# Kernel tuning notes

Hardware: AMD Instinct MI355X
Metric: run time of the kernel (lower is better)

## Reference

```python
import jax, jax.numpy as jnp
import numpy as np
from jax import lax

E = 8          # num_experts
L1 = 1024      # input feature dim
L2 = 15        # hidden 1 (l1 outputs L2+1, last channel is residual)
L3 = 32        # hidden 2
RF = 32        # router features per perspective
AUX_ALPHA = 0.01
Z_ALPHA = 0.001
LOAD_FLOOR = 0.05
LOAD_CAP = 0.5
TEACHER_ALPHA = 0.5  # _teacher_alpha buffer (epoch 0, no annealing)


def setup_inputs() -> dict:
    key = jax.random.key(0)
    ks = jax.random.split(key, 12)
    B = 32768
    s = 0.05
    return {
        "x": jax.random.normal(ks[0], (B, L1), dtype=jnp.float32),
        "ls_indices": jax.random.randint(ks[1], (B,), 0, E),
        "router_w": jax.random.normal(ks[2], (E, 2 * RF), dtype=jnp.float32) * 0.1,
        "router_b": jnp.zeros((E,), dtype=jnp.float32),
        "l1_w": jax.random.normal(ks[3], (E * (L2 + 1), L1), dtype=jnp.float32) * s,
        "l1_fw": jax.random.normal(ks[4], (L2 + 1, L1), dtype=jnp.float32) * s,
        "l1_b": jax.random.normal(ks[5], (E * (L2 + 1),), dtype=jnp.float32) * s,
        "l1_fb": jax.random.normal(ks[6], (L2 + 1,), dtype=jnp.float32) * s,
        "l2_w": jax.random.normal(ks[7], (E * L3, 2 * L2), dtype=jnp.float32) * s,
        "l2_b": jax.random.normal(ks[8], (E * L3,), dtype=jnp.float32) * s,
        "out_w": jax.random.normal(ks[9], (E * 1, L3), dtype=jnp.float32) * s,
        "out_b": jnp.zeros((E * 1,), dtype=jnp.float32),
    }


def _forward(x, ls_indices, router_w, router_b, l1_w, l1_fw, l1_b, l1_fb,
             l2_w, l2_b, out_w, out_b):
    B = x.shape[0]
    half = x.shape[1] // 2

    # ---- router ----
    router_input = jnp.concatenate([x[:, :RF], x[:, half:half + RF]], axis=1)  # (B, 64)
    gate_logits = router_input @ router_w.T + router_b                          # (B, E)
    logp = jax.nn.log_softmax(gate_logits, axis=-1)
    gate_probs = jnp.exp(logp)
    expert_indices = jnp.argmax(gate_logits, axis=-1)                           # (B,)

    target_prob = jnp.take_along_axis(gate_probs, ls_indices[:, None], axis=1).mean()
    bucket_agreement = (expert_indices == ls_indices).astype(gate_probs.dtype).mean()
    teacher_ce = -jnp.take_along_axis(logp, ls_indices[:, None], axis=1).mean()

    fraction_routed = jnp.bincount(expert_indices, length=E).astype(gate_probs.dtype) / B
    avg_gate_prob = gate_probs.mean(axis=0)
    load_estimate = avg_gate_prob + lax.stop_gradient(fraction_routed - avg_gate_prob)
    load_floor_loss = jnp.square(jax.nn.relu(LOAD_FLOOR - load_estimate)).mean()
    load_cap_loss = jnp.square(jax.nn.relu(load_estimate - LOAD_CAP)).mean()
    aux_loss = load_floor_loss + load_cap_loss
    z_loss = jnp.square(jax.scipy.special.logsumexp(gate_logits, axis=-1)).mean()
    router_loss = AUX_ALPHA * aux_loss + Z_ALPHA * z_loss + TEACHER_ALPHA * teacher_ce

    # ---- all-experts MLP (3 batched GEMMs, clamp/square fusion path) ----
    w1 = (l1_w + jnp.tile(l1_fw, (E, 1))).reshape(E, L2 + 1, L1)
    b1 = (l1_b + jnp.tile(l1_fb, E)).reshape(E, L2 + 1)
    w2 = l2_w.reshape(E, L3, 2 * L2)
    b2 = l2_b.reshape(E, L3)
    w3 = out_w.reshape(E, 1, L3)
    b3 = out_b.reshape(E, 1)

    l1c = jnp.einsum('bi,eoi->beo', x, w1) + b1          # (B, E, L2+1)
    l1x, l1x_out = l1c[..., :L2], l1c[..., L2:]          # (B,E,L2), (B,E,1)
    act = jnp.clip(jnp.concatenate([l1x * l1x * (255.0 / 256.0), l1x], axis=2), 0.0, 1.0)
    l2c = jnp.einsum('bei,eoi->beo', act, w2) + b2       # (B, E, L3)
    l2x = jnp.clip(l2c, 0.0, 1.0)
    l3c = jnp.einsum('bei,eoi->beo', l2x, w3) + b3       # (B, E, 1)
    all_out = l3c + l1x_out                              # (B, E, 1)

    # route by argmax expert
    sel = jnp.take_along_axis(all_out, expert_indices[:, None, None], axis=1).squeeze(1)  # (B,1)
    # training-mode straight-through gate scaling (value-preserving)
    gate_prob = jnp.take_along_axis(gate_probs, expert_indices[:, None], axis=1)
    sel = sel * (1.0 + gate_prob - lax.stop_gradient(gate_prob))

    return (sel, router_loss, aux_loss, z_loss, teacher_ce,
            fraction_routed, avg_gate_prob, target_prob, bucket_agreement)


def reference(x, ls_indices, router_w, router_b, l1_w, l1_fw, l1_b, l1_fb,
              l2_w, l2_b, out_w, out_b):
    return _forward(x, ls_indices, router_w, router_b, l1_w, l1_fw, l1_b, l1_fb,
                    l2_w, l2_b, out_w, out_b)
```

## Files before the change

kernel.cpp:

```cpp
#include <hip/hip_runtime.h>
#include <math.h>


#define NE 8
#define NL1 1024
#define NB 32768
#define NCH 512
#define NTOK 32

#define WS_W1C    0
#define WS_B1C    131072
#define WS_COUNTS 131200
#define WS_PART   131208
#define WS_PMAX   132744
#define WS_SORTED 165512

typedef __attribute__((ext_vector_type(4))) float f32x4;
typedef __attribute__((ext_vector_type(8))) short bf16x8;
typedef __attribute__((ext_vector_type(4))) unsigned u32x4;

__device__ __forceinline__ float clamp01(float v) { return fminf(fmaxf(v, 0.0f), 1.0f); }

__device__ __forceinline__ bf16x8 cvt8(float4 lo, float4 hi) {
  unsigned p0, p1, p2, p3;
  asm("v_cvt_pk_bf16_f32 %0, %1, %2" : "=v"(p0) : "v"(lo.x), "v"(lo.y));
  asm("v_cvt_pk_bf16_f32 %0, %1, %2" : "=v"(p1) : "v"(lo.z), "v"(lo.w));
  asm("v_cvt_pk_bf16_f32 %0, %1, %2" : "=v"(p2) : "v"(hi.x), "v"(hi.y));
  asm("v_cvt_pk_bf16_f32 %0, %1, %2" : "=v"(p3) : "v"(hi.z), "v"(hi.w));
  u32x4 u; u.x = p0; u.y = p1; u.z = p2; u.w = p3;
  return __builtin_bit_cast(bf16x8, u);
}

__global__ __launch_bounds__(256) void k_prep(const float* __restrict__ l1_w,
                                              const float* __restrict__ l1_fw,
                                              const float* __restrict__ l1_b,
                                              const float* __restrict__ l1_fb,
                                              float* __restrict__ ws) {
  const int r = blockIdx.x;
  const int t = threadIdx.x;
  const float* src  = l1_w + r * NL1;
  const float* fsrc = l1_fw + (r & 15) * NL1;
  float* dst = ws + WS_W1C + r * NL1;
#pragma unroll
  for (int k = 0; k < 4; ++k) {
    const int i = t + k * 256;
    dst[i] = src[i] + fsrc[i];
  }
  if (r == 0) {
    if (t < 128) ws[WS_B1C + t] = l1_b[t] + l1_fb[t & 15];
    if (t >= 128 && t < 136) ((int*)ws)[WS_COUNTS + (t - 128)] = 0;
  }
}

__device__ __forceinline__ float wsum(float v) {
#pragma unroll
  for (int m = 32; m >= 1; m >>= 1) v += __shfl_xor(v, m, 64);
  return v;
}

__global__ __launch_bounds__(256) void k_router(const float* __restrict__ x,
                                                const int* __restrict__ ls,
                                                const float* __restrict__ rw,
                                                const float* __restrict__ rb,
                                                float* __restrict__ ws) {
  __shared__ float part[4][12];
  __shared__ int hist[NE];
  __shared__ int hbase[NE];
  const int t = threadIdx.x;
  const int w = t >> 6;
  const int b = blockIdx.x * 256 + t;
  if (t < NE) hist[t] = 0;
  __syncthreads();

  float ri[64];
  const float4* xr = (const float4*)(x + (size_t)b * NL1);
#pragma unroll
  for (int q = 0; q < 8; ++q) {
    float4 v = xr[q];
    ri[q * 4 + 0] = v.x; ri[q * 4 + 1] = v.y; ri[q * 4 + 2] = v.z; ri[q * 4 + 3] = v.w;
  }
#pragma unroll
  for (int q = 0; q < 8; ++q) {
    float4 v = xr[128 + q];
    ri[32 + q * 4 + 0] = v.x; ri[32 + q * 4 + 1] = v.y; ri[32 + q * 4 + 2] = v.z; ri[32 + q * 4 + 3] = v.w;
  }

  float logits[NE];
#pragma unroll
  for (int e = 0; e < NE; ++e) {
    float s = rb[e];
    const float* wv = rw + e * 64;
#pragma unroll
    for (int k = 0; k < 64; ++k) s = fmaf(ri[k], wv[k], s);
    logits[e] = s;
  }

  float m = logits[0]; int am = 0;
#pragma unroll
  for (int e = 1; e < NE; ++e) { if (logits[e] > m) { m = logits[e]; am = e; } }
  float se = 0.0f;
#pragma unroll
  for (int e = 0; e < NE; ++e) se += expf(logits[e] - m);
  const float lse = m + logf(se);
  float p[NE];
#pragma unroll
  for (int e = 0; e < NE; ++e) p[e] = expf(logits[e] - lse);

  const int lsb = ls[b];
  float tp = 0.0f, lls = 0.0f, psel = 0.0f;
#pragma unroll
  for (int e = 0; e < NE; ++e) {
    tp   = (e == lsb) ? p[e] : tp;
    lls  = (e == lsb) ? logits[e] : lls;
    psel = (e == am)  ? p[e] : psel;
  }
  const float agree = (am == lsb) ? 1.0f : 0.0f;
  const float tce = lse - lls;
  const float z = lse * lse;

  ws[WS_PMAX + b] = psel;

  int* wsI = (int*)ws;
  const int lpos = atomicAdd(&hist[am], 1);

  const float sA = wsum(tp), sB = wsum(agree), sC = wsum(tce), sD = wsum(z);
  const float q0 = wsum(p[0]), q1 = wsum(p[1]), q2 = wsum(p[2]), q3 = wsum(p[3]);
  const float q4 = wsum(p[4]), q5 = wsum(p[5]), q6 = wsum(p[6]), q7 = wsum(p[7]);
  if ((t & 63) == 0) {
    part[w][0] = sA; part[w][1] = sB; part[w][2]  = sC; part[w][3]  = sD;
    part[w][4] = q0; part[w][5] = q1; part[w][6]  = q2; part[w][7]  = q3;
    part[w][8] = q4; part[w][9] = q5; part[w][10] = q6; part[w][11] = q7;
  }
  __syncthreads();
  if (t < 12) ws[WS_PART + blockIdx.x * 12 + t] =
      (part[0][t] + part[1][t]) + (part[2][t] + part[3][t]);
  if (t < NE) hbase[t] = atomicAdd(&wsI[WS_COUNTS + t], hist[t]);
  __syncthreads();
  wsI[WS_SORTED + am * NB + hbase[am] + lpos] = b;
}

__global__ void k_finalize(const float* __restrict__ ws, float* __restrict__ out) {
  __shared__ float red[12][16];
  const int t = threadIdx.x;
  if (t < 192) {
    const int s = t >> 4, j = t & 15;
    float v = 0.0f;
#pragma unroll
    for (int m = 0; m < 8; ++m) v += ws[WS_PART + (j + 16 * m) * 12 + s];
    red[s][j] = v;
  }
  __syncthreads();
  if (t == 0) {
    float st[12];
#pragma unroll
    for (int s = 0; s < 12; ++s) {
      float v = 0.0f;
#pragma unroll
      for (int j = 0; j < 16; ++j) v += red[s][j];
      st[s] = v;
    }
    const float invB = 1.0f / 32768.0f;
    const int* wsI = (const int*)ws;
    float aux_floor = 0.0f, aux_cap = 0.0f;
#pragma unroll
    for (int e = 0; e < NE; ++e) {
      const float frac = (float)wsI[WS_COUNTS + e] * invB;
      const float avg  = st[4 + e] * invB;
      const float le = avg + (frac - avg);
      const float f = fmaxf(0.05f - le, 0.0f);
      const float c = fmaxf(le - 0.5f, 0.0f);
      aux_floor += f * f;
      aux_cap   += c * c;
      out[32772 + e] = frac;
      out[32780 + e] = avg;
    }
    const float aux = aux_floor * 0.125f + aux_cap * 0.125f;
    const float zl  = st[3] * invB;
    const float tce = st[2] * invB;
    out[32768] = 0.01f * aux + 0.001f * zl + 0.5f * tce;
    out[32769] = aux;
    out[32770] = zl;
    out[32771] = tce;
    out[32788] = st[0] * invB;
    out[32789] = st[1] * invB;
  }
}

__global__ __launch_bounds__(256) void k_expert(const float* __restrict__ x,
                                                const float* __restrict__ ws,
                                                const float* __restrict__ l2_w,
                                                const float* __restrict__ l2_b,
                                                const float* __restrict__ out_w,
                                                const float* __restrict__ out_b,
                                                float* __restrict__ out) {
  __shared__ float lds[8192];
  const int t = threadIdx.x;
  const int l = t & 63;
  const int w = t >> 6;
  const int bid = blockIdx.x;
  const int e = bid >> 9;
  const int c = bid & 511;
  const int* wsI = (const int*)ws;
  const int n = wsI[WS_COUNTS + e];
  const int start = c * NTOK;
  if (start >= n) return;

  const int g = l >> 4;
  const int r0 = l & 15;
  const int r1 = r0 + 16;

  const float* We = ws + WS_W1C + e * 16 * NL1;
  const float* Wr = We + r0 * NL1 + 256 * w + 8 * g;
  bf16x8 bfrag[8];
#pragma unroll
  for (int st2 = 0; st2 < 8; ++st2) {
    const float4 blo = *(const float4*)&Wr[32 * st2];
    const float4 bhi = *(const float4*)&Wr[32 * st2 + 4];
    bfrag[st2] = cvt8(blo, bhi);
  }

  const int lam = l & 31;
  const int lh  = l >> 5;
  const float* srcp[4];
#pragma unroll
  for (int j = 0; j < 4; ++j) {
    const int tl = 8 * w + 2 * j + lh;
    int pos = start + tl; if (pos > n - 1) pos = n - 1;
    const int tokid = wsI[WS_SORTED + e * NB + pos];
    const int cc = (4 * lam) ^ (tl << 2);
    srcp[j] = x + (size_t)tokid * NL1 + 256 * (cc >> 5) + (cc & 31);
  }

  const int q0 = (8 * w + 2 * g) ^ r0;
  const int q1 = (8 * w + 2 * g) ^ r1;
  const int a0lo = r0 * 128 + 4 * q0,        a0hi = r0 * 128 + 4 * (q0 ^ 1);
  const int a1lo = r1 * 128 + 4 * q1,        a1hi = r1 * 128 + 4 * (q1 ^ 1);

#define STAGE(buf, tau) do {                                                    \
  _Pragma("unroll")                                                             \
  for (int j = 0; j < 4; ++j) {                                                 \
    __builtin_amdgcn_global_load_lds(                                           \
        (const __attribute__((address_space(1))) void*)(srcp[j] + 32 * (tau)),  \
        (__attribute__((address_space(3))) void*)&lds[(buf) * 4096 + w * 1024 + j * 256], \
        16, 0, 0);                                                              \
  } } while (0)

#define COMPUTE(buf, tau) do {                                                  \
    const float* Lp = &lds[(buf) * 4096];                                       \
    const float4 v0l = *(const float4*)&Lp[a0lo];                               \
    const float4 v0h = *(const float4*)&Lp[a0hi];                               \
    const float4 v1l = *(const float4*)&Lp[a1lo];                               \
    const float4 v1h = *(const float4*)&Lp[a1hi];                               \
    acc0 = __builtin_amdgcn_mfma_f32_16x16x32_bf16(cvt8(v0l, v0h), bfrag[tau], acc0, 0, 0, 0); \
    acc1 = __builtin_amdgcn_mfma_f32_16x16x32_bf16(cvt8(v1l, v1h), bfrag[tau], acc1, 0, 0, 0); \
  } while (0)

  f32x4 acc0 = {0.f, 0.f, 0.f, 0.f};
  f32x4 acc1 = {0.f, 0.f, 0.f, 0.f};

  STAGE(0, 0);
#pragma unroll
  for (int tau = 0; tau < 8; ++tau) {
    if (tau < 7) {
      STAGE((tau + 1) & 1, tau + 1);
      asm volatile("s_waitcnt vmcnt(4)" ::: "memory");
    } else {
      asm volatile("s_waitcnt vmcnt(0)" ::: "memory");
    }
    __builtin_amdgcn_sched_barrier(0);
    __builtin_amdgcn_s_barrier();
    __builtin_amdgcn_sched_barrier(0);
    COMPUTE(tau & 1, tau);
    __builtin_amdgcn_sched_barrier(0);
    __builtin_amdgcn_s_barrier();
    __builtin_amdgcn_sched_barrier(0);
  }
#undef STAGE
#undef COMPUTE

  __syncthreads();
#pragma unroll
  for (int r = 0; r < 4; ++r) {
    const int tk0 = 4 * (l >> 4) + r;
    lds[w * 544 + tk0 * 17 + (l & 15)]        = acc0[r];
    lds[w * 544 + (16 + tk0) * 17 + (l & 15)] = acc1[r];
  }
  __syncthreads();
#pragma unroll
  for (int pi = 0; pi < 2; ++pi) {
    const int p = t + pi * 256;
    const int tok = p >> 4, o = p & 15;
    float v = (lds[0 * 544 + tok * 17 + o] + lds[1 * 544 + tok * 17 + o]) +
              (lds[2 * 544 + tok * 17 + o] + lds[3 * 544 + tok * 17 + o]);
    v += ws[WS_B1C + e * 16 + o];
    lds[2176 + tok * 17 + o] = v;
  }
  __syncthreads();

  if (t < NTOK) {
    const bool valid = (start + t) < n;
    int pos = start + t; if (pos > n - 1) pos = n - 1;
    const int tokid = wsI[WS_SORTED + e * NB + pos];
    float tot[16];
#pragma unroll
    for (int o = 0; o < 16; ++o) tot[o] = lds[2176 + t * 17 + o];

    float act[30];
#pragma unroll
    for (int j = 0; j < 15; ++j) {
      const float v = tot[j];
      act[j]      = clamp01(v * v * (255.0f / 256.0f));
      act[15 + j] = clamp01(v);
    }
    float y = out_b[e];
    const float* w2r = l2_w + e * 32 * 30;
    const float* w3r = out_w + e * 32;
#pragma unroll 4
    for (int m2 = 0; m2 < 32; ++m2) {
      float s2 = l2_b[e * 32 + m2];
#pragma unroll
      for (int j = 0; j < 30; ++j) s2 = fmaf(act[j], w2r[m2 * 30 + j], s2);
      s2 = clamp01(s2);
      y = fmaf(s2, w3r[m2], y);
    }
    float sel = y + tot[15];
    const float pg = ws[WS_PMAX + tokid];
    sel *= (1.0f + pg) - pg;
    if (valid) out[tokid] = sel;
  }
}

extern "C" void kernel_launch(void* const* d_in, const int* in_sizes, int n_in,
                              void* d_out, int out_size, void* d_ws, size_t ws_size,
                              hipStream_t stream) {
  const float* x     = (const float*)d_in[0];
  const int*   ls    = (const int*)d_in[1];
  const float* rw    = (const float*)d_in[2];
  const float* rb    = (const float*)d_in[3];
  const float* l1_w  = (const float*)d_in[4];
  const float* l1_fw = (const float*)d_in[5];
  const float* l1_b  = (const float*)d_in[6];
  const float* l1_fb = (const float*)d_in[7];
  const float* l2_w  = (const float*)d_in[8];
  const float* l2_b  = (const float*)d_in[9];
  const float* out_w = (const float*)d_in[10];
  const float* out_b = (const float*)d_in[11];
  float* out = (float*)d_out;
  float* ws  = (float*)d_ws;

  k_prep<<<dim3(128), dim3(256), 0, stream>>>(l1_w, l1_fw, l1_b, l1_fb, ws);
  k_router<<<dim3(128), dim3(256), 0, stream>>>(x, ls, rw, rb, ws);
  k_finalize<<<dim3(1), dim3(256), 0, stream>>>(ws, out);
  k_expert<<<dim3(4096), dim3(256), 0, stream>>>(x, ws, l2_w, l2_b, out_w, out_b, out);
}
```

Baseline: 58.33 us.

## Fold weight prep and finalize into expert kernel, restructure K-split with triple-buffered LDS

Removes the separate weight-combine prep kernel by having each expert block add l1_w and l1_fw on the fly while building its bf16 B fragments. It also folds the finalize reduction into an extra block of the expert grid, cutting launch overhead. The main loop is reorganized so each wave handles 16 tokens over half of K, using a per-wave triple-buffered LDS pipeline without block-wide barriers. The trade-off is that every block re-reads the two weight matrices instead of a precombined copy, and each wave holds more B-fragment registers.

```diff
diff --git a/kernel.cpp b/kernel.cpp
--- a/kernel.cpp
+++ b/kernel.cpp
@@ -8,12 +8,10 @@
 #define NCH 512
 #define NTOK 32
 
-#define WS_W1C    0
-#define WS_B1C    131072
-#define WS_COUNTS 131200
-#define WS_PART   131208
-#define WS_PMAX   132744
-#define WS_SORTED 165512
+#define WS_COUNTS 0
+#define WS_PART   8
+#define WS_PMAX   1544
+#define WS_SORTED 34312
 
 typedef __attribute__((ext_vector_type(4))) float f32x4;
 typedef __attribute__((ext_vector_type(8))) short bf16x8;
@@ -31,25 +29,8 @@
   return __builtin_bit_cast(bf16x8, u);
 }
 
-__global__ __launch_bounds__(256) void k_prep(const float* __restrict__ l1_w,
-                                              const float* __restrict__ l1_fw,
-                                              const float* __restrict__ l1_b,
-                                              const float* __restrict__ l1_fb,
-                                              float* __restrict__ ws) {
-  const int r = blockIdx.x;
-  const int t = threadIdx.x;
-  const float* src  = l1_w + r * NL1;
-  const float* fsrc = l1_fw + (r & 15) * NL1;
-  float* dst = ws + WS_W1C + r * NL1;
-#pragma unroll
-  for (int k = 0; k < 4; ++k) {
-    const int i = t + k * 256;
-    dst[i] = src[i] + fsrc[i];
-  }
-  if (r == 0) {
-    if (t < 128) ws[WS_B1C + t] = l1_b[t] + l1_fb[t & 15];
-    if (t >= 128 && t < 136) ((int*)ws)[WS_COUNTS + (t - 128)] = 0;
-  }
+__global__ void k_zero(int* __restrict__ c) {
+  if (threadIdx.x < NE) c[threadIdx.x] = 0;
 }
 
 __device__ __forceinline__ float wsum(float v) {
@@ -139,161 +120,156 @@
   wsI[WS_SORTED + am * NB + hbase[am] + lpos] = b;
 }
 
-__global__ void k_finalize(const float* __restrict__ ws, float* __restrict__ out) {
-  __shared__ float red[12][16];
-  const int t = threadIdx.x;
-  if (t < 192) {
-    const int s = t >> 4, j = t & 15;
-    float v = 0.0f;
-#pragma unroll
-    for (int m = 0; m < 8; ++m) v += ws[WS_PART + (j + 16 * m) * 12 + s];
-    red[s][j] = v;
-  }
-  __syncthreads();
-  if (t == 0) {
-    float st[12];
-#pragma unroll
-    for (int s = 0; s < 12; ++s) {
-      float v = 0.0f;
-#pragma unroll
-      for (int j = 0; j < 16; ++j) v += red[s][j];
-      st[s] = v;
-    }
-    const float invB = 1.0f / 32768.0f;
-    const int* wsI = (const int*)ws;
-    float aux_floor = 0.0f, aux_cap = 0.0f;
-#pragma unroll
-    for (int e = 0; e < NE; ++e) {
-      const float frac = (float)wsI[WS_COUNTS + e] * invB;
-      const float avg  = st[4 + e] * invB;
-      const float le = avg + (frac - avg);
-      const float f = fmaxf(0.05f - le, 0.0f);
-      const float c = fmaxf(le - 0.5f, 0.0f);
-      aux_floor += f * f;
-      aux_cap   += c * c;
-      out[32772 + e] = frac;
-      out[32780 + e] = avg;
-    }
-    const float aux = aux_floor * 0.125f + aux_cap * 0.125f;
-    const float zl  = st[3] * invB;
-    const float tce = st[2] * invB;
-    out[32768] = 0.01f * aux + 0.001f * zl + 0.5f * tce;
-    out[32769] = aux;
-    out[32770] = zl;
-    out[32771] = tce;
-    out[32788] = st[0] * invB;
-    out[32789] = st[1] * invB;
-  }
-}
-
 __global__ __launch_bounds__(256) void k_expert(const float* __restrict__ x,
                                                 const float* __restrict__ ws,
+                                                const float* __restrict__ l1_w,
+                                                const float* __restrict__ l1_fw,
+                                                const float* __restrict__ l1_b,
+                                                const float* __restrict__ l1_fb,
                                                 const float* __restrict__ l2_w,
                                                 const float* __restrict__ l2_b,
                                                 const float* __restrict__ out_w,
                                                 const float* __restrict__ out_b,
                                                 float* __restrict__ out) {
-  __shared__ float lds[8192];
+  __shared__ float lds[6144];
   const int t = threadIdx.x;
-  const int l = t & 63;
-  const int w = t >> 6;
   const int bid = blockIdx.x;
+  const int* wsI = (const int*)ws;
+
+  if (bid == NE * NCH) {
+    if (t < 192) {
+      const int s = t >> 4, j = t & 15;
+      float v = 0.0f;
+#pragma unroll
+      for (int m = 0; m < 8; ++m) v += ws[WS_PART + (j + 16 * m) * 12 + s];
+      lds[s * 16 + j] = v;
+    }
+    __syncthreads();
+    if (t == 0) {
+      float st[12];
+#pragma unroll
+      for (int s = 0; s < 12; ++s) {
+        float v = 0.0f;
+#pragma unroll
+        for (int j = 0; j < 16; ++j) v += lds[s * 16 + j];
+        st[s] = v;
+      }
+      const float invB = 1.0f / 32768.0f;
+      float aux_floor = 0.0f, aux_cap = 0.0f;
+#pragma unroll
+      for (int e = 0; e < NE; ++e) {
+        const float frac = (float)wsI[WS_COUNTS + e] * invB;
+        const float avg  = st[4 + e] * invB;
+        const float le = avg + (frac - avg);
+        const float f = fmaxf(0.05f - le, 0.0f);
+        const float c = fmaxf(le - 0.5f, 0.0f);
+        aux_floor += f * f;
+        aux_cap   += c * c;
+        out[32772 + e] = frac;
+        out[32780 + e] = avg;
+      }
+      const float aux = aux_floor * 0.125f + aux_cap * 0.125f;
+      const float zl  = st[3] * invB;
+      const float tce = st[2] * invB;
+      out[32768] = 0.01f * aux + 0.001f * zl + 0.5f * tce;
+      out[32769] = aux;
+      out[32770] = zl;
+      out[32771] = tce;
+      out[32788] = st[0] * invB;
+      out[32789] = st[1] * invB;
+    }
+    return;
+  }
+
   const int e = bid >> 9;
   const int c = bid & 511;
-  const int* wsI = (const int*)ws;
   const int n = wsI[WS_COUNTS + e];
   const int start = c * NTOK;
   if (start >= n) return;
 
+  const int l = t & 63;
+  const int w = t >> 6;
+  const int tw = w >> 1;
+  const int kw = w & 1;
   const int g = l >> 4;
-  const int r0 = l & 15;
-  const int r1 = r0 + 16;
-
-  const float* We = ws + WS_W1C + e * 16 * NL1;
-  const float* Wr = We + r0 * NL1 + 256 * w + 8 * g;
-  bf16x8 bfrag[8];
-#pragma unroll
-  for (int st2 = 0; st2 < 8; ++st2) {
-    const float4 blo = *(const float4*)&Wr[32 * st2];
-    const float4 bhi = *(const float4*)&Wr[32 * st2 + 4];
-    bfrag[st2] = cvt8(blo, bhi);
-  }
-
-  const int lam = l & 31;
-  const int lh  = l >> 5;
-  const float* srcp[4];
-#pragma unroll
-  for (int j = 0; j < 4; ++j) {
-    const int tl = 8 * w + 2 * j + lh;
-    int pos = start + tl; if (pos > n - 1) pos = n - 1;
+  const int r = l & 15;
+
+  const float* wr = l1_w  + (size_t)(e * 16 + r) * NL1 + kw * 512 + 8 * g;
+  const float* fr = l1_fw + (size_t)r * NL1            + kw * 512 + 8 * g;
+  bf16x8 bfrag[16];
+#pragma unroll
+  for (int st2 = 0; st2 < 16; ++st2) {
+    const float4 wlo = *(const float4*)&wr[32 * st2];
+    const float4 whi = *(const float4*)&wr[32 * st2 + 4];
+    const float4 flo = *(const float4*)&fr[32 * st2];
+    const float4 fhi = *(const float4*)&fr[32 * st2 + 4];
+    float4 lo, hi;
+    lo.x = wlo.x + flo.x; lo.y = wlo.y + flo.y; lo.z = wlo.z + flo.z; lo.w = wlo.w + flo.w;
+    hi.x = whi.x + fhi.x; hi.y = whi.y + fhi.y; hi.z = whi.z + fhi.z; hi.w = whi.w + fhi.w;
+    bfrag[st2] = cvt8(lo, hi);
+  }
+
+  const float* srcp[2];
+#pragma unroll
+  for (int j = 0; j < 2; ++j) {
+    const int row16 = 8 * j + (l >> 3);
+    int pos = start + 16 * tw + row16; if (pos > n - 1) pos = n - 1;
     const int tokid = wsI[WS_SORTED + e * NB + pos];
-    const int cc = (4 * lam) ^ (tl << 2);
-    srcp[j] = x + (size_t)tokid * NL1 + 256 * (cc >> 5) + (cc & 31);
-  }
-
-  const int q0 = (8 * w + 2 * g) ^ r0;
-  const int q1 = (8 * w + 2 * g) ^ r1;
-  const int a0lo = r0 * 128 + 4 * q0,        a0hi = r0 * 128 + 4 * (q0 ^ 1);
-  const int a1lo = r1 * 128 + 4 * q1,        a1hi = r1 * 128 + 4 * (q1 ^ 1);
+    const int col0 = kw * 512 + 4 * ((l & 7) ^ (row16 & 7));
+    srcp[j] = x + (size_t)tokid * NL1 + col0;
+  }
+
+  const int p0 = (2 * g) ^ (r & 7);
+  const float* abase_lo = &lds[w * 1536 + r * 32 + 4 * p0];
+  const float* abase_hi = &lds[w * 1536 + r * 32 + 4 * (p0 ^ 1)];
 
 #define STAGE(buf, tau) do {                                                    \
   _Pragma("unroll")                                                             \
-  for (int j = 0; j < 4; ++j) {                                                 \
+  for (int j = 0; j < 2; ++j) {                                                 \
     __builtin_amdgcn_global_load_lds(                                           \
         (const __attribute__((address_space(1))) void*)(srcp[j] + 32 * (tau)),  \
-        (__attribute__((address_space(3))) void*)&lds[(buf) * 4096 + w * 1024 + j * 256], \
+        (__attribute__((address_space(3))) void*)&lds[w * 1536 + (buf) * 512 + j * 256], \
         16, 0, 0);                                                              \
   } } while (0)
 
 #define COMPUTE(buf, tau) do {                                                  \
-    const float* Lp = &lds[(buf) * 4096];                                       \
-    const float4 v0l = *(const float4*)&Lp[a0lo];                               \
-    const float4 v0h = *(const float4*)&Lp[a0hi];                               \
-    const float4 v1l = *(const float4*)&Lp[a1lo];                               \
-    const float4 v1h = *(const float4*)&Lp[a1hi];                               \
-    acc0 = __builtin_amdgcn_mfma_f32_16x16x32_bf16(cvt8(v0l, v0h), bfrag[tau], acc0, 0, 0, 0); \
-    acc1 = __builtin_amdgcn_mfma_f32_16x16x32_bf16(cvt8(v1l, v1h), bfrag[tau], acc1, 0, 0, 0); \
+    const float4 vlo = *(const float4*)(abase_lo + (buf) * 512);                \
+    const float4 vhi = *(const float4*)(abase_hi + (buf) * 512);                \
+    acc = __builtin_amdgcn_mfma_f32_16x16x32_bf16(cvt8(vlo, vhi), bfrag[tau], acc, 0, 0, 0); \
   } while (0)
 
-  f32x4 acc0 = {0.f, 0.f, 0.f, 0.f};
-  f32x4 acc1 = {0.f, 0.f, 0.f, 0.f};
-
+  f32x4 acc = {0.f, 0.f, 0.f, 0.f};
+
+  asm volatile("s_waitcnt vmcnt(0)" ::: "memory");
+  __builtin_amdgcn_sched_barrier(0);
   STAGE(0, 0);
-#pragma unroll
-  for (int tau = 0; tau < 8; ++tau) {
-    if (tau < 7) {
-      STAGE((tau + 1) & 1, tau + 1);
-      asm volatile("s_waitcnt vmcnt(4)" ::: "memory");
-    } else {
-      asm volatile("s_waitcnt vmcnt(0)" ::: "memory");
-    }
+  STAGE(1, 1);
+#pragma unroll
+  for (int tau = 0; tau < 16; ++tau) {
     __builtin_amdgcn_sched_barrier(0);
-    __builtin_amdgcn_s_barrier();
-    __builtin_amdgcn_sched_barrier(0);
-    COMPUTE(tau & 1, tau);
-    __builtin_amdgcn_sched_barrier(0);
-    __builtin_amdgcn_s_barrier();
-    __builtin_amdgcn_sched_barrier(0);
+    if (tau < 14) STAGE((tau + 2) % 3, tau + 2);
+    if (tau < 14)       { asm volatile("s_waitcnt vmcnt(4)" ::: "memory"); }
+    else if (tau == 14) { asm volatile("s_waitcnt vmcnt(2)" ::: "memory"); }
+    else                { asm volatile("s_waitcnt vmcnt(0)" ::: "memory"); }
+    COMPUTE(tau % 3, tau);
   }
 #undef STAGE
 #undef COMPUTE
 
   __syncthreads();
 #pragma unroll
-  for (int r = 0; r < 4; ++r) {
-    const int tk0 = 4 * (l >> 4) + r;
-    lds[w * 544 + tk0 * 17 + (l & 15)]        = acc0[r];
-    lds[w * 544 + (16 + tk0) * 17 + (l & 15)] = acc1[r];
+  for (int q = 0; q < 4; ++q) {
+    lds[w * 272 + (4 * g + q) * 17 + r] = acc[q];
   }
   __syncthreads();
 #pragma unroll
   for (int pi = 0; pi < 2; ++pi) {
     const int p = t + pi * 256;
-    const int tok = p >> 4, o = p & 15;
-    float v = (lds[0 * 544 + tok * 17 + o] + lds[1 * 544 + tok * 17 + o]) +
-              (lds[2 * 544 + tok * 17 + o] + lds[3 * 544 + tok * 17 + o]);
-    v += ws[WS_B1C + e * 16 + o];
-    lds[2176 + tok * 17 + o] = v;
+    const int tok32 = p >> 4, o = p & 15;
+    const int twq = tok32 >> 4, tk = tok32 & 15;
+    float v = lds[(2 * twq) * 272 + tk * 17 + o] + lds[(2 * twq + 1) * 272 + tk * 17 + o];
+    v += l1_b[e * 16 + o] + l1_fb[o];
+    lds[1088 + tok32 * 17 + o] = v;
   }
   __syncthreads();
 
@@ -303,7 +279,7 @@
     const int tokid = wsI[WS_SORTED + e * NB + pos];
     float tot[16];
 #pragma unroll
-    for (int o = 0; o < 16; ++o) tot[o] = lds[2176 + t * 17 + o];
+    for (int o = 0; o < 16; ++o) tot[o] = lds[1088 + t * 17 + o];
 
     float act[30];
 #pragma unroll
@@ -348,8 +324,8 @@
   float* out = (float*)d_out;
   float* ws  = (float*)d_ws;
 
-  k_prep<<<dim3(128), dim3(256), 0, stream>>>(l1_w, l1_fw, l1_b, l1_fb, ws);
+  k_zero<<<dim3(1), dim3(64), 0, stream>>>((int*)ws + WS_COUNTS);
   k_router<<<dim3(128), dim3(256), 0, stream>>>(x, ls, rw, rb, ws);
-  k_finalize<<<dim3(1), dim3(256), 0, stream>>>(ws, out);
-  k_expert<<<dim3(4096), dim3(256), 0, stream>>>(x, ws, l2_w, l2_b, out_w, out_b, out);
-}
+  k_expert<<<dim3(NE * NCH + 1), dim3(256), 0, stream>>>(
+      x, ws, l1_w, l1_fw, l1_b, l1_fb, l2_w, l2_b, out_w, out_b, out);
+}
```

After: 87.89 us. +50.7%, slower.
